# Kernel tuning notes

Measured on AMD Instinct MI355X. Metric: run time of the kernel, lower is better.

Reference implementation:

```python
import jax, jax.numpy as jnp
import numpy as np

D_MODEL = 1024
N_HEADS = 16
H_DIM = D_MODEL // N_HEADS
B, T = 2, 2048


def setup_inputs() -> dict:
    key = jax.random.key(0)
    ks = jax.random.split(key, 11)
    s = 1.0 / np.sqrt(D_MODEL)
    inp = {
        "q": jax.random.normal(ks[0], (B, T, D_MODEL), dtype=jnp.float32),
        "k": jax.random.normal(ks[1], (B, T, D_MODEL), dtype=jnp.float32),
        "v": jax.random.normal(ks[2], (B, T, D_MODEL), dtype=jnp.float32),
        "Wq": jax.random.normal(ks[3], (D_MODEL, D_MODEL), dtype=jnp.float32) * s,
        "bq": jnp.zeros((D_MODEL,), dtype=jnp.float32),
        "Wk": jax.random.normal(ks[4], (D_MODEL, D_MODEL), dtype=jnp.float32) * s,
        "bk": jnp.zeros((D_MODEL,), dtype=jnp.float32),
        "Wv": jax.random.normal(ks[5], (D_MODEL, D_MODEL), dtype=jnp.float32) * s,
        "bv": jnp.zeros((D_MODEL,), dtype=jnp.float32),
        "Wo": jax.random.normal(ks[6], (D_MODEL, D_MODEL), dtype=jnp.float32) * s,
        "bo": jnp.zeros((D_MODEL,), dtype=jnp.float32),
    }
    return inp


def reference(q, k, v, Wq, bq, Wk, bk, Wv, bv, Wo, bo):
    # Linear projections (W stored so that y = x @ W + b)
    qp = q @ Wq + bq  # [B,T,D]
    kp = k @ Wk + bk
    vp = v @ Wv + bv
    Bz, Tz, _ = qp.shape
    # [B,T,H,h] -> [B,H,T,h]
    qh = qp.reshape(Bz, Tz, N_HEADS, H_DIM).transpose(0, 2, 1, 3)
    kh = kp.reshape(Bz, Tz, N_HEADS, H_DIM).transpose(0, 2, 1, 3)
    vh = vp.reshape(Bz, Tz, N_HEADS, H_DIM).transpose(0, 2, 1, 3)
    scale = 1.0 / np.sqrt(H_DIM).astype(np.float32)
    scores = jnp.einsum('bhqd,bhkd->bhqk', qh, kh) * scale  # [B,H,T,T]
    attn = jax.nn.softmax(scores, axis=-1)  # dropout is identity in eval
    ctx = jnp.einsum('bhqk,bhkd->bhqd', attn, vh)  # [B,H,T,h]
    ctx = ctx.transpose(0, 2, 1, 3).reshape(Bz, Tz, D_MODEL)
    return ctx @ Wo + bo
```

## Files before the change

kernel.cpp:

```cpp
#include <hip/hip_runtime.h>

typedef __bf16 bf16x8 __attribute__((ext_vector_type(8)));
typedef float f32x4 __attribute__((ext_vector_type(4)));
typedef float f32x16 __attribute__((ext_vector_type(16)));
typedef unsigned short u16;
typedef unsigned short u16x8 __attribute__((ext_vector_type(8)));
typedef unsigned int u32;

#define MROWS 4096
#define DMODEL 1024
#define TSEQ 2048

__device__ __forceinline__ u32 bfr(float x) {
    u32 u = __float_as_uint(x);
    return (u + 0x7FFFu + ((u >> 16) & 1u)) >> 16;
}
__device__ __forceinline__ u32 pk2(float lo, float hi) { return bfr(lo) | (bfr(hi) << 16); }

__device__ __forceinline__ u32 cvtpk(float lo, float hi) {
    u32 r;
    asm("v_cvt_pk_bf16_f32 %0, %1, %2" : "=v"(r) : "v"(lo), "v"(hi));
    return r;
}

__device__ __forceinline__ void gl_lds16(const void* g, void* l) {
    __builtin_amdgcn_global_load_lds(
        (const __attribute__((address_space(1))) unsigned int*)g,
        (__attribute__((address_space(3))) unsigned int*)l, 16, 0, 0);
}

__global__ __launch_bounds__(256) void cvt_x(const float* __restrict__ q,
                                             const float* __restrict__ k,
                                             const float* __restrict__ v,
                                             u16* __restrict__ X) {
    int z = blockIdx.y;
    const float* src = (z == 0) ? q : (z == 1) ? k : v;
    size_t idx = ((size_t)blockIdx.x * 256 + threadIdx.x) * 8;
    const float4* s4 = (const float4*)(src + idx);
    float4 a = s4[0], b = s4[1];
    uint4 r;
    r.x = pk2(a.x, a.y); r.y = pk2(a.z, a.w);
    r.z = pk2(b.x, b.y); r.w = pk2(b.z, b.w);
    *(uint4*)(X + (size_t)z * 4194304 + idx) = r;
}

__global__ __launch_bounds__(256) void cvt_w(const float* __restrict__ w0,
                                             const float* __restrict__ w1,
                                             const float* __restrict__ w2,
                                             const float* __restrict__ w3,
                                             u16* __restrict__ Wt) {
    int z = blockIdx.z;
    const float* W = (z == 0) ? w0 : (z == 1) ? w1 : (z == 2) ? w2 : w3;
    u16* dst = Wt + (size_t)z * 1048576;
    __shared__ float tile[32][33];
    int n0 = blockIdx.x * 32, k0 = blockIdx.y * 32;
    int tx = threadIdx.x & 31, ty = threadIdx.x >> 5;
#pragma unroll
    for (int r = 0; r < 4; r++) {
        int row = ty + r * 8;
        tile[row][tx] = W[(size_t)(k0 + row) * DMODEL + n0 + tx];
    }
    __syncthreads();
#pragma unroll
    for (int r = 0; r < 4; r++) {
        int row = ty + r * 8;
        dst[(size_t)(n0 + row) * DMODEL + k0 + tx] = (u16)bfr(tile[tx][row]);
    }
}

template <int OUT_BF16>
__global__ __launch_bounds__(256) void gemm4p(const u16* __restrict__ Abase,
                                              const u16* __restrict__ Btbase,
                                              const float* __restrict__ b0,
                                              const float* __restrict__ b1,
                                              const float* __restrict__ b2,
                                              void* __restrict__ Cout, int ldc) {
    int z = blockIdx.z;
    const u16* A  = Abase + (size_t)z * 4194304;
    const u16* Bt = Btbase + (size_t)z * 1048576;
    const float* bias = (z == 0) ? b0 : (z == 1) ? b1 : b2;
    int id = blockIdx.y * 8 + blockIdx.x;
    int swz = (id & 7) * 32 + (id >> 3);
    int brow = (swz >> 3) * 128, bcol = (swz & 7) * 128;
    int t = threadIdx.x, lane = t & 63, wid = t >> 6;
    int wr = wid >> 1, wc = wid & 1;
    int l15 = lane & 15, g = lane >> 4;
    int sw = (l15 >> 1) & 3;

    __shared__ __align__(16) u16 SH[32768];

    f32x4 acc[4][4];
#pragma unroll
    for (int i = 0; i < 4; i++)
#pragma unroll
        for (int j = 0; j < 4; j++) acc[i][j] = f32x4{0.f, 0.f, 0.f, 0.f};

    auto stage = [&](int kc) {
        int b = kc & 3;
#pragma unroll
        for (int l = 0; l < 2; l++) {
            int c = l * 256 + t;
            int row = c >> 2, gch = c & 3;
            int gs = gch ^ ((row >> 1) & 3);
            gl_lds16(A + (size_t)(brow + row) * DMODEL + kc * 32 + gs * 8,
                     &SH[b * 4096 + c * 8]);
            gl_lds16(Bt + (size_t)(bcol + row) * DMODEL + kc * 32 + gs * 8,
                     &SH[16384 + b * 4096 + c * 8]);
        }
    };

    auto chunk_body = [&](int kc) {
        const u16* Ab = &SH[(kc & 3) * 4096];
        const u16* Bb = &SH[16384 + (kc & 3) * 4096];
        bf16x8 af[4], bfv[4];
#pragma unroll
        for (int mi = 0; mi < 4; mi++)
            af[mi] = *(const bf16x8*)&Ab[(wr * 64 + mi * 16 + l15) * 32 + ((g ^ sw) * 8)];
#pragma unroll
        for (int nj = 0; nj < 4; nj++)
            bfv[nj] = *(const bf16x8*)&Bb[(wc * 64 + nj * 16 + l15) * 32 + ((g ^ sw) * 8)];
        __builtin_amdgcn_s_setprio(1);
#pragma unroll
        for (int mi = 0; mi < 4; mi++)
#pragma unroll
            for (int nj = 0; nj < 4; nj++)
                acc[mi][nj] = __builtin_amdgcn_mfma_f32_16x16x32_bf16(af[mi], bfv[nj], acc[mi][nj], 0, 0, 0);
        __builtin_amdgcn_s_setprio(0);
    };

    stage(0); stage(1); stage(2);

    for (int kc = 0; kc < 31; ++kc) {
        asm volatile("s_waitcnt vmcnt(4)" ::: "memory");
        __builtin_amdgcn_s_barrier();
        __builtin_amdgcn_sched_barrier(0);
        if (kc < 29) stage(kc + 3);
        chunk_body(kc);
    }
    asm volatile("s_waitcnt vmcnt(0)" ::: "memory");
    __builtin_amdgcn_s_barrier();
    __builtin_amdgcn_sched_barrier(0);
    chunk_body(31);

#pragma unroll
    for (int nj = 0; nj < 4; nj++) {
        int n = bcol + wc * 64 + nj * 16 + l15;
        float bv = bias[n];
#pragma unroll
        for (int mi = 0; mi < 4; mi++) {
#pragma unroll
            for (int r = 0; r < 4; r++) {
                int row = brow + wr * 64 + mi * 16 + g * 4 + r;
                float val = acc[mi][nj][r] + bv;
                if (OUT_BF16) {
                    if (z == 0) val *= 0.18033688f;
                    ((u16*)Cout)[(size_t)row * ldc + z * DMODEL + n] = (u16)bfr(val);
                } else {
                    ((float*)Cout)[(size_t)row * ldc + n] = val;
                }
            }
        }
    }
}

__global__ __launch_bounds__(512, 1) void attn(const u16* __restrict__ QKV, u16* __restrict__ CTX) {
    int id = blockIdx.y * 8 + blockIdx.x;
    int swz = (id & 7) * 32 + (id >> 3);
    int qt = swz & 7;
    int bh = swz >> 3;
    int head = bh & 15;
    size_t base = (size_t)(bh >> 4) * TSEQ * 3072;
    int t = threadIdx.x;
    int tl = t & 255;
    int grp = t >> 8;
    int lane = t & 63, wid = t >> 6;
    int lw = wid & 3;
    int l31 = lane & 31, hf = lane >> 5;

    __shared__ __align__(16) u16 SH[32768];
    u16* Kg = SH + grp * 16384;
    u16* Vg = SH + grp * 16384 + 8192;

    int qwave = qt * 256 + lw * 64;
    const u16* QpA = QKV + base + (size_t)(qwave + l31) * 3072 + head * 64;
    const u16* QpB = QpA + 32 * 3072;
    bf16x8 qfA[4], qfB[4];
#pragma unroll
    for (int c = 0; c < 4; c++) {
        qfA[c] = *(const bf16x8*)(QpA + c * 16 + hf * 8);
        qfB[c] = *(const bf16x8*)(QpB + c * 16 + hf * 8);
    }

    f32x16 oA0 = {}, oA1 = {}, oB0 = {}, oB1 = {};
    float lA = 0.f, lB = 0.f;

    int vkv = (tl & 31) * 2;
    int vd0 = (tl >> 5) * 8;
    int vslot = (vkv & ~12) | ((vkv & 4) << 1) | ((vkv & 8) >> 1);
    u16x8 vr0, vr1;

    auto stageK = [&](int buf, int kvb) {
#pragma unroll
        for (int i = 0; i < 2; i++) {
            int c = i * 256 + lw * 64 + lane;
            int kv = c >> 3, kc = (c & 7) ^ (kv & 7);
            gl_lds16(QKV + base + (size_t)(kvb * 64 + kv) * 3072 + 1024 + head * 64 + kc * 8,
                     &Kg[buf * 4096 + (i * 256 + lw * 64) * 8]);
        }
    };
    auto loadV = [&](int kvb) {
        const u16* Vp = QKV + base + (size_t)(kvb * 64) * 3072 + 2048 + head * 64;
        vr0 = *(const u16x8*)(Vp + (size_t)vkv * 3072 + vd0);
        vr1 = *(const u16x8*)(Vp + (size_t)(vkv + 1) * 3072 + vd0);
    };
    auto writeV = [&](int buf) {
#pragma unroll
        for (int e = 0; e < 8; e++) {
            int d = vd0 + e;
            int kvs = vslot ^ ((d >> 4) << 4) ^ ((d & 7) << 3);
            u32 p = (u32)vr0[e] | ((u32)vr1[e] << 16);
            *(u32*)&Vg[buf * 4096 + d * 64 + kvs] = p;
        }
    };

    int kvb0 = grp * 16;
    stageK(0, kvb0);
    loadV(kvb0);
    writeV(0);
    __syncthreads();

    int kx = (l31 & 7) * 8;

    for (int j = 0; j < 16; ++j) {
        int cur = j & 1, nxt = cur ^ 1;
        if (j < 15) { stageK(nxt, kvb0 + j + 1); loadV(kvb0 + j + 1); }

        f32x16 s0A = {}, s1A = {}, s0B = {}, s1B = {};
        const u16* kr0 = &Kg[cur * 4096 + l31 * 64];
        const u16* kr1 = kr0 + 32 * 64;
        __builtin_amdgcn_s_setprio(1);
#pragma unroll
        for (int c = 0; c < 4; c++) {
            int slot = ((2 * c + hf) * 8) ^ kx;
            bf16x8 a0 = *(const bf16x8*)(kr0 + slot);
            bf16x8 a1 = *(const bf16x8*)(kr1 + slot);
            s0A = __builtin_amdgcn_mfma_f32_32x32x16_bf16(a0, qfA[c], s0A, 0, 0, 0);
            s1A = __builtin_amdgcn_mfma_f32_32x32x16_bf16(a1, qfA[c], s1A, 0, 0, 0);
            s0B = __builtin_amdgcn_mfma_f32_32x32x16_bf16(a0, qfB[c], s0B, 0, 0, 0);
            s1B = __builtin_amdgcn_mfma_f32_32x32x16_bf16(a1, qfB[c], s1B, 0, 0, 0);
        }
        __builtin_amdgcn_s_setprio(0);

        float p0A[16], p1A[16], p0B[16], p1B[16];
#pragma unroll
        for (int r = 0; r < 16; r++) {
            p0A[r] = __builtin_amdgcn_exp2f(s0A[r]);
            p1A[r] = __builtin_amdgcn_exp2f(s1A[r]);
            p0B[r] = __builtin_amdgcn_exp2f(s0B[r]);
            p1B[r] = __builtin_amdgcn_exp2f(s1B[r]);
        }
        float sa = 0.f, sb = 0.f, sc = 0.f, sd = 0.f;
#pragma unroll
        for (int r = 0; r < 8; r++) {
            sa += p0A[r] + p0A[r + 8];
            sb += p1A[r] + p1A[r + 8];
            sc += p0B[r] + p0B[r + 8];
            sd += p1B[r] + p1B[r + 8];
        }
        lA += sa + sb;
        lB += sc + sd;

        union FragU { u32 u[4]; bf16x8 v; };
        bf16x8 paA[4], paB[4];
        {
            FragU fA, fB2, fC, fD;
#pragma unroll
            for (int w = 0; w < 4; w++) {
                fA.u[w]  = cvtpk(p0A[2 * w],     p0A[2 * w + 1]);
                fB2.u[w] = cvtpk(p0A[8 + 2 * w], p0A[9 + 2 * w]);
                fC.u[w]  = cvtpk(p1A[2 * w],     p1A[2 * w + 1]);
                fD.u[w]  = cvtpk(p1A[8 + 2 * w], p1A[9 + 2 * w]);
            }
            paA[0] = fA.v; paA[1] = fB2.v; paA[2] = fC.v; paA[3] = fD.v;
#pragma unroll
            for (int w = 0; w < 4; w++) {
                fA.u[w]  = cvtpk(p0B[2 * w],     p0B[2 * w + 1]);
                fB2.u[w] = cvtpk(p0B[8 + 2 * w], p0B[9 + 2 * w]);
                fC.u[w]  = cvtpk(p1B[2 * w],     p1B[2 * w + 1]);
                fD.u[w]  = cvtpk(p1B[8 + 2 * w], p1B[9 + 2 * w]);
            }
            paB[0] = fA.v; paB[1] = fB2.v; paB[2] = fC.v; paB[3] = fD.v;
        }

        if (j < 15) writeV(nxt);

        __builtin_amdgcn_s_setprio(1);
#pragma unroll
        for (int kc = 0; kc < 4; kc++) {
            int d0 = l31;
            int sl0 = ((2 * kc + hf) ^ (d0 & 7) ^ ((d0 >> 4) << 1)) * 8;
            bf16x8 v0 = *(const bf16x8*)&Vg[cur * 4096 + d0 * 64 + sl0];
            int d1 = 32 + l31;
            int sl1 = ((2 * kc + hf) ^ (d1 & 7) ^ ((d1 >> 4) << 1)) * 8;
            bf16x8 v1 = *(const bf16x8*)&Vg[cur * 4096 + d1 * 64 + sl1];
            oA0 = __builtin_amdgcn_mfma_f32_32x32x16_bf16(paA[kc], v0, oA0, 0, 0, 0);
            oA1 = __builtin_amdgcn_mfma_f32_32x32x16_bf16(paA[kc], v1, oA1, 0, 0, 0);
            oB0 = __builtin_amdgcn_mfma_f32_32x32x16_bf16(paB[kc], v0, oB0, 0, 0, 0);
            oB1 = __builtin_amdgcn_mfma_f32_32x32x16_bf16(paB[kc], v1, oB1, 0, 0, 0);
        }
        __builtin_amdgcn_s_setprio(0);
        __syncthreads();
    }

    lA += __shfl_xor(lA, 32);
    lB += __shfl_xor(lB, 32);

    float* FB = (float*)SH;
    if (grp == 1) {
#pragma unroll
        for (int r = 0; r < 16; r++) {
            FB[lw * 2048 + r * 64 + lane]        = oA0[r];
            FB[lw * 2048 + 1024 + r * 64 + lane] = oA1[r];
        }
        FB[8192 + lw * 64 + lane] = lA;
    }
    __syncthreads();
    if (grp == 0) {
        float l1 = FB[8192 + lw * 64 + lane];
        float rl = 1.0f / (lA + l1);
#pragma unroll
        for (int r = 0; r < 16; r++) {
            int qr = (r & 3) + 8 * (r >> 2) + 4 * hf;
            float rr = __shfl(rl, qr);
            float po0 = FB[lw * 2048 + r * 64 + lane];
            float po1 = FB[lw * 2048 + 1024 + r * 64 + lane];
            size_t rowoff = ((size_t)(bh >> 4) * TSEQ + qwave + qr) * DMODEL + head * 64;
            CTX[rowoff + l31]      = (u16)bfr((oA0[r] + po0) * rr);
            CTX[rowoff + 32 + l31] = (u16)bfr((oA1[r] + po1) * rr);
        }
    }
    __syncthreads();
    if (grp == 1) {
#pragma unroll
        for (int r = 0; r < 16; r++) {
            FB[lw * 2048 + r * 64 + lane]        = oB0[r];
            FB[lw * 2048 + 1024 + r * 64 + lane] = oB1[r];
        }
        FB[8192 + lw * 64 + lane] = lB;
    }
    __syncthreads();
    if (grp == 0) {
        float l1 = FB[8192 + lw * 64 + lane];
        float rl = 1.0f / (lB + l1);
#pragma unroll
        for (int r = 0; r < 16; r++) {
            int qr = (r & 3) + 8 * (r >> 2) + 4 * hf;
            float rr = __shfl(rl, qr);
            float po0 = FB[lw * 2048 + r * 64 + lane];
            float po1 = FB[lw * 2048 + 1024 + r * 64 + lane];
            size_t rowoff = ((size_t)(bh >> 4) * TSEQ + qwave + 32 + qr) * DMODEL + head * 64;
            CTX[rowoff + l31]      = (u16)bfr((oB0[r] + po0) * rr);
            CTX[rowoff + 32 + l31] = (u16)bfr((oB1[r] + po1) * rr);
        }
    }
}

extern "C" void kernel_launch(void* const* d_in, const int* in_sizes, int n_in,
                              void* d_out, int out_size, void* d_ws, size_t ws_size,
                              hipStream_t stream) {
    const float* q  = (const float*)d_in[0];
    const float* k  = (const float*)d_in[1];
    const float* v  = (const float*)d_in[2];
    const float* Wq = (const float*)d_in[3];
    const float* bq = (const float*)d_in[4];
    const float* Wk = (const float*)d_in[5];
    const float* bk = (const float*)d_in[6];
    const float* Wv = (const float*)d_in[7];
    const float* bv = (const float*)d_in[8];
    const float* Wo = (const float*)d_in[9];
    const float* bo = (const float*)d_in[10];

    char* ws = (char*)d_ws;
    u16* Xbf = (u16*)ws;
    u16* Wt  = (u16*)(ws + 25165824);
    u16* QKV = (u16*)(ws + 25165824 + 8388608);
    u16* CTX = Xbf;

    cvt_x<<<dim3(2048, 3), 256, 0, stream>>>(q, k, v, Xbf);
    cvt_w<<<dim3(32, 32, 4), 256, 0, stream>>>(Wq, Wk, Wv, Wo, Wt);
    gemm4p<1><<<dim3(8, 32, 3), 256, 0, stream>>>(Xbf, Wt, bq, bk, bv, QKV, 3072);
    attn<<<dim3(8, 32), 512, 0, stream>>>(QKV, CTX);
    gemm4p<0><<<dim3(8, 32, 1), 256, 0, stream>>>(CTX, Wt + 3 * 1048576, bo, bo, bo, d_out, 1024);
}
```

Before: 108.5 us.

## Drop intra-block KV split in attention and merge conversion kernels

The attention kernel moves from 512-thread blocks, where two groups split the KV range and combined their partial outputs through shared memory, to 128-thread blocks of two waves. Each block now walks the full KV sequence over 128 query rows, and the grid grows to 512 blocks. This removes the cross-group reduction and its barriers and halves shared memory per block, at the cost of a serial KV loop twice as long per wave. The two fp32-to-bf16 conversion kernels are also fused into one launch to save launch overhead.

```diff
diff --git a/kernel.cpp b/kernel.cpp
--- a/kernel.cpp
+++ b/kernel.cpp
@@ -29,42 +29,45 @@
         (__attribute__((address_space(3))) unsigned int*)l, 16, 0, 0);
 }
 
-__global__ __launch_bounds__(256) void cvt_x(const float* __restrict__ q,
-                                             const float* __restrict__ k,
-                                             const float* __restrict__ v,
-                                             u16* __restrict__ X) {
-    int z = blockIdx.y;
-    const float* src = (z == 0) ? q : (z == 1) ? k : v;
-    size_t idx = ((size_t)blockIdx.x * 256 + threadIdx.x) * 8;
-    const float4* s4 = (const float4*)(src + idx);
-    float4 a = s4[0], b = s4[1];
-    uint4 r;
-    r.x = pk2(a.x, a.y); r.y = pk2(a.z, a.w);
-    r.z = pk2(b.x, b.y); r.w = pk2(b.z, b.w);
-    *(uint4*)(X + (size_t)z * 4194304 + idx) = r;
-}
-
-__global__ __launch_bounds__(256) void cvt_w(const float* __restrict__ w0,
-                                             const float* __restrict__ w1,
-                                             const float* __restrict__ w2,
-                                             const float* __restrict__ w3,
-                                             u16* __restrict__ Wt) {
-    int z = blockIdx.z;
-    const float* W = (z == 0) ? w0 : (z == 1) ? w1 : (z == 2) ? w2 : w3;
-    u16* dst = Wt + (size_t)z * 1048576;
-    __shared__ float tile[32][33];
-    int n0 = blockIdx.x * 32, k0 = blockIdx.y * 32;
-    int tx = threadIdx.x & 31, ty = threadIdx.x >> 5;
-#pragma unroll
-    for (int r = 0; r < 4; r++) {
-        int row = ty + r * 8;
-        tile[row][tx] = W[(size_t)(k0 + row) * DMODEL + n0 + tx];
-    }
-    __syncthreads();
-#pragma unroll
-    for (int r = 0; r < 4; r++) {
-        int row = ty + r * 8;
-        dst[(size_t)(n0 + row) * DMODEL + k0 + tx] = (u16)bfr(tile[tx][row]);
+__global__ __launch_bounds__(256) void cvt_all(const float* __restrict__ q,
+                                               const float* __restrict__ k,
+                                               const float* __restrict__ v,
+                                               const float* __restrict__ w0,
+                                               const float* __restrict__ w1,
+                                               const float* __restrict__ w2,
+                                               const float* __restrict__ w3,
+                                               u16* __restrict__ X,
+                                               u16* __restrict__ Wt) {
+    int id = blockIdx.x;
+    if (id < 6144) {
+        int z = id >> 11, bx = id & 2047;
+        const float* src = (z == 0) ? q : (z == 1) ? k : v;
+        size_t idx = ((size_t)bx * 256 + threadIdx.x) * 8;
+        const float4* s4 = (const float4*)(src + idx);
+        float4 a = s4[0], b = s4[1];
+        uint4 r;
+        r.x = pk2(a.x, a.y); r.y = pk2(a.z, a.w);
+        r.z = pk2(b.x, b.y); r.w = pk2(b.z, b.w);
+        *(uint4*)(X + (size_t)z * 4194304 + idx) = r;
+    } else {
+        int w = id - 6144;
+        int z = w >> 10, rem = w & 1023;
+        const float* W = (z == 0) ? w0 : (z == 1) ? w1 : (z == 2) ? w2 : w3;
+        u16* dst = Wt + (size_t)z * 1048576;
+        __shared__ float tile[32][33];
+        int n0 = (rem & 31) * 32, k0 = (rem >> 5) * 32;
+        int tx = threadIdx.x & 31, ty = threadIdx.x >> 5;
+#pragma unroll
+        for (int r = 0; r < 4; r++) {
+            int row = ty + r * 8;
+            tile[row][tx] = W[(size_t)(k0 + row) * DMODEL + n0 + tx];
+        }
+        __syncthreads();
+#pragma unroll
+        for (int r = 0; r < 4; r++) {
+            int row = ty + r * 8;
+            dst[(size_t)(n0 + row) * DMODEL + k0 + tx] = (u16)bfr(tile[tx][row]);
+        }
     }
 }
 
@@ -163,25 +166,24 @@
     }
 }
 
-__global__ __launch_bounds__(512, 1) void attn(const u16* __restrict__ QKV, u16* __restrict__ CTX) {
-    int id = blockIdx.y * 8 + blockIdx.x;
-    int swz = (id & 7) * 32 + (id >> 3);
-    int qt = swz & 7;
-    int bh = swz >> 3;
+__global__ __launch_bounds__(128, 1) void attn(const u16* __restrict__ QKV, u16* __restrict__ CTX) {
+    int id = blockIdx.y * 16 + blockIdx.x;
+    int swz = (id & 7) * 64 + (id >> 3);
+    int qt = swz & 15;
+    int bh = swz >> 4;
     int head = bh & 15;
-    size_t base = (size_t)(bh >> 4) * TSEQ * 3072;
+    int bz = bh >> 4;
+    size_t base = (size_t)bz * TSEQ * 3072;
     int t = threadIdx.x;
-    int tl = t & 255;
-    int grp = t >> 8;
-    int lane = t & 63, wid = t >> 6;
-    int lw = wid & 3;
+    int lane = t & 63;
+    int lw = t >> 6;
     int l31 = lane & 31, hf = lane >> 5;
 
-    __shared__ __align__(16) u16 SH[32768];
-    u16* Kg = SH + grp * 16384;
-    u16* Vg = SH + grp * 16384 + 8192;
-
-    int qwave = qt * 256 + lw * 64;
+    __shared__ __align__(16) u16 SH[16384];
+    u16* Kg = SH;
+    u16* Vg = SH + 8192;
+
+    int qwave = qt * 128 + lw * 64;
     const u16* QpA = QKV + base + (size_t)(qwave + l31) * 3072 + head * 64;
     const u16* QpB = QpA + 32 * 3072;
     bf16x8 qfA[4], qfB[4];
@@ -194,46 +196,51 @@
     f32x16 oA0 = {}, oA1 = {}, oB0 = {}, oB1 = {};
     float lA = 0.f, lB = 0.f;
 
-    int vkv = (tl & 31) * 2;
-    int vd0 = (tl >> 5) * 8;
+    int vkv = (t & 31) * 2;
+    int vdh = (t >> 5) * 16;
     int vslot = (vkv & ~12) | ((vkv & 4) << 1) | ((vkv & 8) >> 1);
-    u16x8 vr0, vr1;
+    u16x8 vr0a, vr1a, vr0b, vr1b;
 
     auto stageK = [&](int buf, int kvb) {
 #pragma unroll
-        for (int i = 0; i < 2; i++) {
-            int c = i * 256 + lw * 64 + lane;
+        for (int i = 0; i < 4; i++) {
+            int c = i * 128 + lw * 64 + lane;
             int kv = c >> 3, kc = (c & 7) ^ (kv & 7);
             gl_lds16(QKV + base + (size_t)(kvb * 64 + kv) * 3072 + 1024 + head * 64 + kc * 8,
-                     &Kg[buf * 4096 + (i * 256 + lw * 64) * 8]);
+                     &Kg[buf * 4096 + (i * 128 + lw * 64) * 8]);
         }
     };
     auto loadV = [&](int kvb) {
         const u16* Vp = QKV + base + (size_t)(kvb * 64) * 3072 + 2048 + head * 64;
-        vr0 = *(const u16x8*)(Vp + (size_t)vkv * 3072 + vd0);
-        vr1 = *(const u16x8*)(Vp + (size_t)(vkv + 1) * 3072 + vd0);
+        const u16* p0 = Vp + (size_t)vkv * 3072;
+        const u16* p1 = Vp + (size_t)(vkv + 1) * 3072;
+        vr0a = *(const u16x8*)(p0 + vdh);
+        vr1a = *(const u16x8*)(p1 + vdh);
+        vr0b = *(const u16x8*)(p0 + vdh + 8);
+        vr1b = *(const u16x8*)(p1 + vdh + 8);
     };
     auto writeV = [&](int buf) {
 #pragma unroll
         for (int e = 0; e < 8; e++) {
-            int d = vd0 + e;
+            int d = vdh + e;
             int kvs = vslot ^ ((d >> 4) << 4) ^ ((d & 7) << 3);
-            u32 p = (u32)vr0[e] | ((u32)vr1[e] << 16);
-            *(u32*)&Vg[buf * 4096 + d * 64 + kvs] = p;
-        }
-    };
-
-    int kvb0 = grp * 16;
-    stageK(0, kvb0);
-    loadV(kvb0);
+            *(u32*)&Vg[buf * 4096 + d * 64 + kvs] = (u32)vr0a[e] | ((u32)vr1a[e] << 16);
+            int d2 = vdh + 8 + e;
+            int kvs2 = vslot ^ ((d2 >> 4) << 4) ^ ((d2 & 7) << 3);
+            *(u32*)&Vg[buf * 4096 + d2 * 64 + kvs2] = (u32)vr0b[e] | ((u32)vr1b[e] << 16);
+        }
+    };
+
+    stageK(0, 0);
+    loadV(0);
     writeV(0);
     __syncthreads();
 
     int kx = (l31 & 7) * 8;
 
-    for (int j = 0; j < 16; ++j) {
+    for (int j = 0; j < 32; ++j) {
         int cur = j & 1, nxt = cur ^ 1;
-        if (j < 15) { stageK(nxt, kvb0 + j + 1); loadV(kvb0 + j + 1); }
+        if (j < 31) { stageK(nxt, j + 1); loadV(j + 1); }
 
         f32x16 s0A = {}, s1A = {}, s0B = {}, s1B = {};
         const u16* kr0 = &Kg[cur * 4096 + l31 * 64];
@@ -292,7 +299,7 @@
             paB[0] = fA.v; paB[1] = fB2.v; paB[2] = fC.v; paB[3] = fD.v;
         }
 
-        if (j < 15) writeV(nxt);
+        if (j < 31) writeV(nxt);
 
         __builtin_amdgcn_s_setprio(1);
 #pragma unroll
@@ -314,54 +321,20 @@
 
     lA += __shfl_xor(lA, 32);
     lB += __shfl_xor(lB, 32);
-
-    float* FB = (float*)SH;
-    if (grp == 1) {
-#pragma unroll
-        for (int r = 0; r < 16; r++) {
-            FB[lw * 2048 + r * 64 + lane]        = oA0[r];
-            FB[lw * 2048 + 1024 + r * 64 + lane] = oA1[r];
-        }
-        FB[8192 + lw * 64 + lane] = lA;
-    }
-    __syncthreads();
-    if (grp == 0) {
-        float l1 = FB[8192 + lw * 64 + lane];
-        float rl = 1.0f / (lA + l1);
-#pragma unroll
-        for (int r = 0; r < 16; r++) {
-            int qr = (r & 3) + 8 * (r >> 2) + 4 * hf;
-            float rr = __shfl(rl, qr);
-            float po0 = FB[lw * 2048 + r * 64 + lane];
-            float po1 = FB[lw * 2048 + 1024 + r * 64 + lane];
-            size_t rowoff = ((size_t)(bh >> 4) * TSEQ + qwave + qr) * DMODEL + head * 64;
-            CTX[rowoff + l31]      = (u16)bfr((oA0[r] + po0) * rr);
-            CTX[rowoff + 32 + l31] = (u16)bfr((oA1[r] + po1) * rr);
-        }
-    }
-    __syncthreads();
-    if (grp == 1) {
-#pragma unroll
-        for (int r = 0; r < 16; r++) {
-            FB[lw * 2048 + r * 64 + lane]        = oB0[r];
-            FB[lw * 2048 + 1024 + r * 64 + lane] = oB1[r];
-        }
-        FB[8192 + lw * 64 + lane] = lB;
-    }
-    __syncthreads();
-    if (grp == 0) {
-        float l1 = FB[8192 + lw * 64 + lane];
-        float rl = 1.0f / (lB + l1);
-#pragma unroll
-        for (int r = 0; r < 16; r++) {
-            int qr = (r & 3) + 8 * (r >> 2) + 4 * hf;
-            float rr = __shfl(rl, qr);
-            float po0 = FB[lw * 2048 + r * 64 + lane];
-            float po1 = FB[lw * 2048 + 1024 + r * 64 + lane];
-            size_t rowoff = ((size_t)(bh >> 4) * TSEQ + qwave + 32 + qr) * DMODEL + head * 64;
-            CTX[rowoff + l31]      = (u16)bfr((oB0[r] + po0) * rr);
-            CTX[rowoff + 32 + l31] = (u16)bfr((oB1[r] + po1) * rr);
-        }
+    float rlA = 1.0f / lA;
+    float rlB = 1.0f / lB;
+
+#pragma unroll
+    for (int r = 0; r < 16; r++) {
+        int qr = (r & 3) + 8 * (r >> 2) + 4 * hf;
+        float ra = __shfl(rlA, qr);
+        size_t rowoff = ((size_t)bz * TSEQ + qwave + qr) * DMODEL + head * 64;
+        CTX[rowoff + l31]      = (u16)bfr(oA0[r] * ra);
+        CTX[rowoff + 32 + l31] = (u16)bfr(oA1[r] * ra);
+        float rb = __shfl(rlB, qr);
+        size_t rowoff2 = ((size_t)bz * TSEQ + qwave + 32 + qr) * DMODEL + head * 64;
+        CTX[rowoff2 + l31]      = (u16)bfr(oB0[r] * rb);
+        CTX[rowoff2 + 32 + l31] = (u16)bfr(oB1[r] * rb);
     }
 }
 
@@ -386,9 +359,8 @@
     u16* QKV = (u16*)(ws + 25165824 + 8388608);
     u16* CTX = Xbf;
 
-    cvt_x<<<dim3(2048, 3), 256, 0, stream>>>(q, k, v, Xbf);
-    cvt_w<<<dim3(32, 32, 4), 256, 0, stream>>>(Wq, Wk, Wv, Wo, Wt);
+    cvt_all<<<10240, 256, 0, stream>>>(q, k, v, Wq, Wk, Wv, Wo, Xbf, Wt);
     gemm4p<1><<<dim3(8, 32, 3), 256, 0, stream>>>(Xbf, Wt, bq, bk, bv, QKV, 3072);
-    attn<<<dim3(8, 32), 512, 0, stream>>>(QKV, CTX);
+    attn<<<dim3(16, 32), 128, 0, stream>>>(QKV, CTX);
     gemm4p<0><<<dim3(8, 32, 1), 256, 0, stream>>>(CTX, Wt + 3 * 1048576, bo, bo, bo, d_out, 1024);
 }
```

New measurement: 124.4 us. 14.7% more time.
